# Kernel optimization log

Hardware: AMD Instinct MI355X
Metric: run time of the kernel (lower is better)

## Reference

```python
import jax, jax.numpy as jnp
import numpy as np

DIM = 2048
N_HEADS = 16
HEAD_DIM = DIM // N_HEADS
B, S = 2, 2048


def apply_rotary(x, cos, sin):
    # x: [..., dim]; cos/sin broadcast to [..., dim//2]
    # even/odd interleaved rotation, matching the torch ::2 / 1::2 indexing
    xe = x[..., 0::2]
    xo = x[..., 1::2]
    oe = xe * cos - xo * sin
    oo = xo * cos + xe * sin
    return jnp.stack([oe, oo], axis=-1).reshape(x.shape)


def setup_inputs() -> dict:
    key = jax.random.key(0)
    ks = jax.random.split(key, 12)
    scale = 1.0 / np.sqrt(DIM)
    x = jax.random.normal(ks[0], (B, S, DIM), dtype=jnp.float32)
    cos = jax.random.normal(ks[1], (S, DIM // 2), dtype=jnp.float32)
    sin = jax.random.normal(ks[2], (S, DIM // 2), dtype=jnp.float32)
    mask = jnp.zeros((1, 1, S, S), dtype=jnp.float32)
    Wq = jax.random.normal(ks[3], (DIM, DIM), dtype=jnp.float32) * scale
    bq = jnp.zeros((DIM,), dtype=jnp.float32)
    Wk = jax.random.normal(ks[4], (DIM, DIM), dtype=jnp.float32) * scale
    bk = jnp.zeros((DIM,), dtype=jnp.float32)
    Wv = jax.random.normal(ks[5], (DIM, DIM), dtype=jnp.float32) * scale
    bv = jnp.zeros((DIM,), dtype=jnp.float32)
    Wo = jax.random.normal(ks[6], (DIM, DIM), dtype=jnp.float32) * scale
    bo = jnp.zeros((DIM,), dtype=jnp.float32)
    return {"x": x, "cos": cos, "sin": sin, "mask": mask,
            "Wq": Wq, "bq": bq, "Wk": Wk, "bk": bk,
            "Wv": Wv, "bv": bv, "Wo": Wo, "bo": bo}


def reference(x, cos, sin, mask, Wq, bq, Wk, bk, Wv, bv, Wo, bo):
    # Linear projections (torch nn.Linear: y = x @ W.T + b)
    q = jnp.einsum('bsd,ed->bse', x, Wq) + bq
    k = jnp.einsum('bsd,ed->bse', x, Wk) + bk
    v = jnp.einsum('bsd,ed->bse', x, Wv) + bv
    # RoPE on full dim, then split into heads (faithful to source ordering)
    q = apply_rotary(q, cos, sin).reshape(B, S, N_HEADS, HEAD_DIM)
    k = apply_rotary(k, cos, sin).reshape(B, S, N_HEADS, HEAD_DIM)
    v = v.reshape(B, S, N_HEADS, HEAD_DIM)
    scale = 1.0 / jnp.sqrt(jnp.float32(HEAD_DIM))
    attn = jnp.einsum('bqhd,bkhd->bhqk', q, k) * scale  # [B,H,S,S]
    attn = attn + mask
    attn = jax.nn.softmax(attn, axis=-1)
    out = jnp.einsum('bhqk,bkhd->bqhd', attn, v).reshape(B, S, DIM)
    return jnp.einsum('bsd,ed->bse', out, Wo) + bo
```

## Files before the change

### kernel.cpp

```cpp
#include <hip/hip_runtime.h>

#define DIM   2048
#define SLEN  2048
#define BATCH 2
#define NHEAD 16
#define HDIM  128
#define MROWS (BATCH*SLEN)

typedef __attribute__((ext_vector_type(8))) __bf16 bf16x8;
typedef __attribute__((ext_vector_type(4))) float  f32x4;
typedef __attribute__((ext_vector_type(8))) unsigned short u16x8;
typedef __attribute__((ext_vector_type(4))) unsigned short u16x4;

__device__ __forceinline__ unsigned short f2bf(float f) {
  union { float f; unsigned u; } v; v.f = f;
  unsigned r = v.u + 0x7FFFu + ((v.u >> 16) & 1u);
  return (unsigned short)(r >> 16);
}
__device__ __forceinline__ float bf2f(unsigned short h) {
  union { unsigned u; float f; } v; v.u = ((unsigned)h) << 16;
  return v.f;
}
__device__ __forceinline__ void gload16(const void* g, void* l) {
  __builtin_amdgcn_global_load_lds(
      (const __attribute__((address_space(1))) void*)g,
      (__attribute__((address_space(3))) void*)l, 16, 0, 0);
}

__global__ __launch_bounds__(256) void conv_f32_bf16(
    const float* __restrict__ in, unsigned short* __restrict__ out, int n4) {
  int t = blockIdx.x * 256 + threadIdx.x;
  if (t >= n4) return;
  f32x4 v = *(const f32x4*)(in + (size_t)t * 4);
  u16x4 o;
  o[0] = f2bf(v[0]); o[1] = f2bf(v[1]); o[2] = f2bf(v[2]); o[3] = f2bf(v[3]);
  *(u16x4*)(out + (size_t)t * 4) = o;
}

template<int OUT_MODE>
__global__ __launch_bounds__(256) void gemm_bt(
    const unsigned short* __restrict__ A,
    const unsigned short* __restrict__ Bw,
    const float* __restrict__ bias,
    void* __restrict__ Cout, int M, int N, int K)
{
  __shared__ __align__(16) unsigned short As[128][32];
  __shared__ __align__(16) unsigned short Bs[128][32];
  const int tid  = threadIdx.x;
  const int lane = tid & 63;
  const int wid  = tid >> 6;
  const int wr   = wid >> 1, wc = wid & 1;
  const int lrow = lane >> 4, lcol = lane & 15;
  const int row0 = blockIdx.x * 128, col0 = blockIdx.y * 128;

  f32x4 acc[4][4] = {};

  const unsigned short* Ablk = A  + (size_t)row0 * K;
  const unsigned short* Bblk = Bw + (size_t)col0 * K;
  char* AsB = (char*)&As[0][0];
  char* BsB = (char*)&Bs[0][0];

  for (int k0 = 0; k0 < K; k0 += 32) {
#pragma unroll
    for (int r = 0; r < 2; ++r) {
      int f = r * 256 + tid;
      gload16(Ablk + (size_t)(f >> 2) * K + k0 + (f & 3) * 8, AsB + (r * 256 + wid * 64) * 16);
      gload16(Bblk + (size_t)(f >> 2) * K + k0 + (f & 3) * 8, BsB + (r * 256 + wid * 64) * 16);
    }
    __syncthreads();
    bf16x8 af[4], bfv[4];
#pragma unroll
    for (int m = 0; m < 4; ++m)
      af[m] = *(const bf16x8*)&As[wr * 64 + m * 16 + lcol][lrow * 8];
#pragma unroll
    for (int n = 0; n < 4; ++n)
      bfv[n] = *(const bf16x8*)&Bs[wc * 64 + n * 16 + lcol][lrow * 8];
#pragma unroll
    for (int m = 0; m < 4; ++m)
#pragma unroll
      for (int n = 0; n < 4; ++n)
        acc[m][n] = __builtin_amdgcn_mfma_f32_16x16x32_bf16(af[m], bfv[n], acc[m][n], 0, 0, 0);
    __syncthreads();
  }

#pragma unroll
  for (int m = 0; m < 4; ++m) {
#pragma unroll
    for (int n = 0; n < 4; ++n) {
      int col = col0 + wc * 64 + n * 16 + lcol;
      float bv = bias[col];
      if (OUT_MODE == 2) {
        int row = row0 + wr * 64 + m * 16 + lrow * 4;
        u16x4 o;
#pragma unroll
        for (int j = 0; j < 4; ++j) o[j] = f2bf(acc[m][n][j] + bv);
        *(u16x4*)((unsigned short*)Cout +
                  ((size_t)((row >> 11) * DIM + col)) * SLEN + (row & (SLEN - 1))) = o;
      } else {
#pragma unroll
        for (int j = 0; j < 4; ++j) {
          int row = row0 + wr * 64 + m * 16 + lrow * 4 + j;
          float val = acc[m][n][j] + bv;
          if (OUT_MODE == 1) ((unsigned short*)Cout)[(size_t)row * N + col] = f2bf(val);
          else               ((float*)Cout)[(size_t)row * N + col] = val;
        }
      }
    }
  }
}

__global__ __launch_bounds__(256) void rope_inplace(
    unsigned short* __restrict__ q,
    const float* __restrict__ cosT, const float* __restrict__ sinT, float scale) {
  int t   = blockIdx.x * 256 + threadIdx.x;
  int row = t >> 8;
  int e0  = (t & 255) * 8;
  int s   = row & (SLEN - 1);
  unsigned short* p = q + (size_t)row * DIM + e0;
  u16x8 v = *(u16x8*)p;
  f32x4 c  = *(const f32x4*)(cosT + (size_t)s * (DIM / 2) + (e0 >> 1));
  f32x4 sn = *(const f32x4*)(sinT + (size_t)s * (DIM / 2) + (e0 >> 1));
#pragma unroll
  for (int i = 0; i < 4; ++i) {
    float xe = bf2f(v[2 * i]), xo = bf2f(v[2 * i + 1]);
    float oe = (xe * c[i] - xo * sn[i]) * scale;
    float oo = (xo * c[i] + xe * sn[i]) * scale;
    v[2 * i] = f2bf(oe); v[2 * i + 1] = f2bf(oo);
  }
  *(u16x8*)p = v;
}

__global__ __launch_bounds__(256) void attn_fwd(
    const unsigned short* __restrict__ Q,
    const unsigned short* __restrict__ Kg,
    const unsigned short* __restrict__ VtG,
    const float* __restrict__ mask,
    unsigned short* __restrict__ O)
{
  __shared__ __align__(16) unsigned short Ks[64][128];
  __shared__ __align__(16) unsigned short Vts[128][64];
  __shared__ __align__(16) unsigned short Ps[4][16][64];

  const int qt = blockIdx.x, h = blockIdx.y, b = blockIdx.z;
  const int tid = threadIdx.x, lane = tid & 63, wid = tid >> 6;
  const int lrow = lane >> 4, lcol = lane & 15;
  const int sx = (lcol & 7) << 4;

  const unsigned short* Qb  = Q  + ((size_t)(b * SLEN + qt * 64)) * DIM + h * HDIM;
  const unsigned short* Kb  = Kg + (size_t)(b * SLEN) * DIM + h * HDIM;
  const unsigned short* Vtb = VtG + ((size_t)(b * DIM + h * HDIM)) * SLEN;
  const float* maskRow = mask + (size_t)(qt * 64 + wid * 16 + lcol) * SLEN;

  bf16x8 qf[4];
#pragma unroll
  for (int kk = 0; kk < 4; ++kk)
    qf[kk] = *(const bf16x8*)(Qb + (size_t)(wid * 16 + lcol) * DIM + kk * 32 + lrow * 8);

  float m_run = -1e30f, l_run = 0.f;
  f32x4 acc_o[8] = {};

  char* KsB  = (char*)&Ks[0][0];
  char* VtsB = (char*)&Vts[0][0];
  char* PsB  = (char*)&Ps[0][0][0];

  for (int kt = 0; kt < SLEN / 64; ++kt) {
    __syncthreads();
#pragma unroll
    for (int r = 0; r < 4; ++r) {
      int L = r * 256 + wid * 64 + lane;
      int krow = L >> 4, kc = (L & 15) ^ (krow & 7);
      gload16(Kb + (size_t)(kt * 64 + krow) * DIM + kc * 8,
              KsB + (size_t)(r * 256 + wid * 64) * 16);
    }
#pragma unroll
    for (int r = 0; r < 4; ++r) {
      int L = r * 256 + wid * 64 + lane;
      int d = L >> 3, vc = (L & 7) ^ (d & 7);
      gload16(Vtb + (size_t)d * SLEN + kt * 64 + vc * 8,
              VtsB + (size_t)(r * 256 + wid * 64) * 16);
    }
    __syncthreads();

    f32x4 sacc[4] = {};
#pragma unroll
    for (int kn = 0; kn < 4; ++kn)
#pragma unroll
      for (int kk = 0; kk < 4; ++kk) {
        bf16x8 kf = *(const bf16x8*)(KsB + (size_t)(kn * 16 + lcol) * 256
                                         + ((kk * 64 + lrow * 16) ^ sx));
        sacc[kn] = __builtin_amdgcn_mfma_f32_16x16x32_bf16(kf, qf[kk], sacc[kn], 0, 0, 0);
      }

    float sv[16];
#pragma unroll
    for (int kn = 0; kn < 4; ++kn) {
      f32x4 mv = *(const f32x4*)(maskRow + kt * 64 + kn * 16 + lrow * 4);
#pragma unroll
      for (int r = 0; r < 4; ++r) sv[kn * 4 + r] = sacc[kn][r] + mv[r];
    }

    float pmax = sv[0];
#pragma unroll
    for (int i = 1; i < 16; ++i) pmax = fmaxf(pmax, sv[i]);
    pmax = fmaxf(pmax, __shfl_xor(pmax, 16, 64));
    pmax = fmaxf(pmax, __shfl_xor(pmax, 32, 64));

    if (!__all(pmax - m_run <= 8.0f)) {
      float mnew = fmaxf(m_run, pmax);
      float alpha = __expf(m_run - mnew);
      m_run = mnew;
      l_run *= alpha;
      float ar[4];
#pragma unroll
      for (int r = 0; r < 4; ++r) ar[r] = __shfl(alpha, lrow * 4 + r, 64);
#pragma unroll
      for (int d = 0; d < 8; ++d) {
        f32x4 t = acc_o[d];
#pragma unroll
        for (int r = 0; r < 4; ++r) t[r] *= ar[r];
        acc_o[d] = t;
      }
    }

    float pv[16];
    float rsum = 0.f;
#pragma unroll
    for (int i = 0; i < 16; ++i) { float pe = __expf(sv[i] - m_run); pv[i] = pe; rsum += pe; }
    rsum += __shfl_xor(rsum, 16, 64);
    rsum += __shfl_xor(rsum, 32, 64);
    l_run += rsum;

#pragma unroll
    for (int kn = 0; kn < 4; ++kn)
#pragma unroll
      for (int r = 0; r < 4; ++r)
        *(unsigned short*)(PsB + wid * 2048 + lcol * 128
                           + ((kn * 32 + (lrow * 4 + r) * 2) ^ sx)) = f2bf(pv[kn * 4 + r]);

    bf16x8 pf[2];
#pragma unroll
    for (int ks = 0; ks < 2; ++ks)
      pf[ks] = *(const bf16x8*)(PsB + wid * 2048 + lcol * 128
                                + ((ks * 64 + lrow * 16) ^ sx));
#pragma unroll
    for (int d = 0; d < 8; ++d)
#pragma unroll
      for (int ks = 0; ks < 2; ++ks) {
        bf16x8 vf = *(const bf16x8*)(VtsB + (size_t)(d * 16 + lcol) * 128
                                          + ((ks * 64 + lrow * 16) ^ sx));
        acc_o[d] = __builtin_amdgcn_mfma_f32_16x16x32_bf16(pf[ks], vf, acc_o[d], 0, 0, 0);
      }
  }

  float linv[4];
#pragma unroll
  for (int r = 0; r < 4; ++r) linv[r] = 1.0f / __shfl(l_run, lrow * 4 + r, 64);
  int orow0 = b * SLEN + qt * 64 + wid * 16 + lrow * 4;
#pragma unroll
  for (int d = 0; d < 8; ++d)
#pragma unroll
    for (int r = 0; r < 4; ++r) {
      float o = acc_o[d][r] * linv[r];
      O[(size_t)(orow0 + r) * DIM + h * HDIM + d * 16 + lcol] = f2bf(o);
    }
}

extern "C" void kernel_launch(void* const* d_in, const int* in_sizes, int n_in,
                              void* d_out, int out_size, void* d_ws, size_t ws_size,
                              hipStream_t stream) {
  const float* x    = (const float*)d_in[0];
  const float* cosT = (const float*)d_in[1];
  const float* sinT = (const float*)d_in[2];
  const float* mask = (const float*)d_in[3];
  const float* Wq   = (const float*)d_in[4];
  const float* bq   = (const float*)d_in[5];
  const float* Wk   = (const float*)d_in[6];
  const float* bk   = (const float*)d_in[7];
  const float* Wv   = (const float*)d_in[8];
  const float* bv   = (const float*)d_in[9];
  const float* Wo   = (const float*)d_in[10];
  const float* bo   = (const float*)d_in[11];

  const size_t MB = 1u << 20;
  if (ws_size < 72 * MB) return;

  char* ws = (char*)d_ws;
  unsigned short* xb = (unsigned short*)(ws);
  unsigned short* qb = (unsigned short*)(ws + 16 * MB);
  unsigned short* kb = (unsigned short*)(ws + 32 * MB);
  unsigned short* Vt = (unsigned short*)(ws + 48 * MB);
  unsigned short* Wb = (unsigned short*)(ws + 64 * MB);
  unsigned short* Ob = xb;

  dim3 gGemm(MROWS / 128, DIM / 128);
  const float scale = 0.08838834764831845f;

  conv_f32_bf16<<<8192, 256, 0, stream>>>(x, xb, (MROWS * DIM) / 4);
  conv_f32_bf16<<<4096, 256, 0, stream>>>(Wq, Wb, (DIM * DIM) / 4);
  gemm_bt<1><<<gGemm, 256, 0, stream>>>(xb, Wb, bq, qb, MROWS, DIM, DIM);
  conv_f32_bf16<<<4096, 256, 0, stream>>>(Wk, Wb, (DIM * DIM) / 4);
  gemm_bt<1><<<gGemm, 256, 0, stream>>>(xb, Wb, bk, kb, MROWS, DIM, DIM);
  conv_f32_bf16<<<4096, 256, 0, stream>>>(Wv, Wb, (DIM * DIM) / 4);
  gemm_bt<2><<<gGemm, 256, 0, stream>>>(xb, Wb, bv, Vt, MROWS, DIM, DIM);
  rope_inplace<<<4096, 256, 0, stream>>>(qb, cosT, sinT, scale);
  rope_inplace<<<4096, 256, 0, stream>>>(kb, cosT, sinT, 1.0f);
  attn_fwd<<<dim3(SLEN / 64, NHEAD, BATCH), 256, 0, stream>>>(qb, kb, Vt, mask, Ob);
  conv_f32_bf16<<<4096, 256, 0, stream>>>(Wo, Wb, (DIM * DIM) / 4);
  gemm_bt<0><<<gGemm, 256, 0, stream>>>(Ob, Wb, bo, d_out, MROWS, DIM, DIM);
}
```

Baseline: 434.8 us.

## Process two 16-row query subtiles per wave in attention to reuse K/V tiles

Each wave in the attention kernel now handles 32 query rows as two 16-row subtiles, so every block covers 128 queries instead of 64 and the grid is halved. Each K and V fragment read from LDS feeds two MFMAs, which halves global K/V loads per query and LDS reads per MFMA. P stores to LDS are also vectorized into 4-element writes. The cost is roughly double the accumulator and softmax-state registers and fewer blocks, which may reduce occupancy (512 blocks on the GPU).

```diff
diff --git a/kernel.cpp b/kernel.cpp
--- a/kernel.cpp
+++ b/kernel.cpp
@@ -139,25 +139,27 @@
 {
   __shared__ __align__(16) unsigned short Ks[64][128];
   __shared__ __align__(16) unsigned short Vts[128][64];
-  __shared__ __align__(16) unsigned short Ps[4][16][64];
+  __shared__ __align__(16) unsigned short Ps[4][32][64];
 
   const int qt = blockIdx.x, h = blockIdx.y, b = blockIdx.z;
   const int tid = threadIdx.x, lane = tid & 63, wid = tid >> 6;
   const int lrow = lane >> 4, lcol = lane & 15;
   const int sx = (lcol & 7) << 4;
 
-  const unsigned short* Qb  = Q  + ((size_t)(b * SLEN + qt * 64)) * DIM + h * HDIM;
+  const unsigned short* Qb  = Q  + ((size_t)(b * SLEN + qt * 128 + wid * 32)) * DIM + h * HDIM;
   const unsigned short* Kb  = Kg + (size_t)(b * SLEN) * DIM + h * HDIM;
   const unsigned short* Vtb = VtG + ((size_t)(b * DIM + h * HDIM)) * SLEN;
-  const float* maskRow = mask + (size_t)(qt * 64 + wid * 16 + lcol) * SLEN;
-
-  bf16x8 qf[4];
-#pragma unroll
-  for (int kk = 0; kk < 4; ++kk)
-    qf[kk] = *(const bf16x8*)(Qb + (size_t)(wid * 16 + lcol) * DIM + kk * 32 + lrow * 8);
-
-  float m_run = -1e30f, l_run = 0.f;
-  f32x4 acc_o[8] = {};
+  const float* mrow0 = mask + (size_t)(qt * 128 + wid * 32 + lcol) * SLEN;
+
+  bf16x8 qf[2][4];
+#pragma unroll
+  for (int qs = 0; qs < 2; ++qs)
+#pragma unroll
+    for (int kk = 0; kk < 4; ++kk)
+      qf[qs][kk] = *(const bf16x8*)(Qb + (size_t)(qs * 16 + lcol) * DIM + kk * 32 + lrow * 8);
+
+  float m_run[2] = {-1e30f, -1e30f}, l_run[2] = {0.f, 0.f};
+  f32x4 acc_o[2][8] = {};
 
   char* KsB  = (char*)&Ks[0][0];
   char* VtsB = (char*)&Vts[0][0];
@@ -181,88 +183,100 @@
     }
     __syncthreads();
 
-    f32x4 sacc[4] = {};
+    f32x4 sacc[2][4] = {};
 #pragma unroll
     for (int kn = 0; kn < 4; ++kn)
 #pragma unroll
       for (int kk = 0; kk < 4; ++kk) {
         bf16x8 kf = *(const bf16x8*)(KsB + (size_t)(kn * 16 + lcol) * 256
                                          + ((kk * 64 + lrow * 16) ^ sx));
-        sacc[kn] = __builtin_amdgcn_mfma_f32_16x16x32_bf16(kf, qf[kk], sacc[kn], 0, 0, 0);
-      }
-
-    float sv[16];
-#pragma unroll
-    for (int kn = 0; kn < 4; ++kn) {
-      f32x4 mv = *(const f32x4*)(maskRow + kt * 64 + kn * 16 + lrow * 4);
-#pragma unroll
-      for (int r = 0; r < 4; ++r) sv[kn * 4 + r] = sacc[kn][r] + mv[r];
-    }
-
-    float pmax = sv[0];
-#pragma unroll
-    for (int i = 1; i < 16; ++i) pmax = fmaxf(pmax, sv[i]);
-    pmax = fmaxf(pmax, __shfl_xor(pmax, 16, 64));
-    pmax = fmaxf(pmax, __shfl_xor(pmax, 32, 64));
-
-    if (!__all(pmax - m_run <= 8.0f)) {
-      float mnew = fmaxf(m_run, pmax);
-      float alpha = __expf(m_run - mnew);
-      m_run = mnew;
-      l_run *= alpha;
-      float ar[4];
-#pragma unroll
-      for (int r = 0; r < 4; ++r) ar[r] = __shfl(alpha, lrow * 4 + r, 64);
-#pragma unroll
-      for (int d = 0; d < 8; ++d) {
-        f32x4 t = acc_o[d];
-#pragma unroll
-        for (int r = 0; r < 4; ++r) t[r] *= ar[r];
-        acc_o[d] = t;
-      }
-    }
-
-    float pv[16];
-    float rsum = 0.f;
-#pragma unroll
-    for (int i = 0; i < 16; ++i) { float pe = __expf(sv[i] - m_run); pv[i] = pe; rsum += pe; }
-    rsum += __shfl_xor(rsum, 16, 64);
-    rsum += __shfl_xor(rsum, 32, 64);
-    l_run += rsum;
-
-#pragma unroll
-    for (int kn = 0; kn < 4; ++kn)
-#pragma unroll
-      for (int r = 0; r < 4; ++r)
-        *(unsigned short*)(PsB + wid * 2048 + lcol * 128
-                           + ((kn * 32 + (lrow * 4 + r) * 2) ^ sx)) = f2bf(pv[kn * 4 + r]);
-
-    bf16x8 pf[2];
-#pragma unroll
-    for (int ks = 0; ks < 2; ++ks)
-      pf[ks] = *(const bf16x8*)(PsB + wid * 2048 + lcol * 128
-                                + ((ks * 64 + lrow * 16) ^ sx));
+        sacc[0][kn] = __builtin_amdgcn_mfma_f32_16x16x32_bf16(kf, qf[0][kk], sacc[0][kn], 0, 0, 0);
+        sacc[1][kn] = __builtin_amdgcn_mfma_f32_16x16x32_bf16(kf, qf[1][kk], sacc[1][kn], 0, 0, 0);
+      }
+
+#pragma unroll
+    for (int qs = 0; qs < 2; ++qs) {
+      float sv[16];
+#pragma unroll
+      for (int kn = 0; kn < 4; ++kn) {
+        f32x4 mv = *(const f32x4*)(mrow0 + (size_t)qs * 16 * SLEN + kt * 64 + kn * 16 + lrow * 4);
+#pragma unroll
+        for (int r = 0; r < 4; ++r) sv[kn * 4 + r] = sacc[qs][kn][r] + mv[r];
+      }
+
+      float pmax = sv[0];
+#pragma unroll
+      for (int i = 1; i < 16; ++i) pmax = fmaxf(pmax, sv[i]);
+      pmax = fmaxf(pmax, __shfl_xor(pmax, 16, 64));
+      pmax = fmaxf(pmax, __shfl_xor(pmax, 32, 64));
+
+      if (!__all(pmax - m_run[qs] <= 8.0f)) {
+        float mnew = fmaxf(m_run[qs], pmax);
+        float alpha = __expf(m_run[qs] - mnew);
+        m_run[qs] = mnew;
+        l_run[qs] *= alpha;
+        float ar[4];
+#pragma unroll
+        for (int r = 0; r < 4; ++r) ar[r] = __shfl(alpha, lrow * 4 + r, 64);
+#pragma unroll
+        for (int d = 0; d < 8; ++d) {
+          f32x4 t = acc_o[qs][d];
+#pragma unroll
+          for (int r = 0; r < 4; ++r) t[r] *= ar[r];
+          acc_o[qs][d] = t;
+        }
+      }
+
+      float pv[16];
+      float rsum = 0.f;
+#pragma unroll
+      for (int i = 0; i < 16; ++i) { float pe = __expf(sv[i] - m_run[qs]); pv[i] = pe; rsum += pe; }
+      rsum += __shfl_xor(rsum, 16, 64);
+      rsum += __shfl_xor(rsum, 32, 64);
+      l_run[qs] += rsum;
+
+#pragma unroll
+      for (int kn = 0; kn < 4; ++kn) {
+        u16x4 o;
+#pragma unroll
+        for (int r = 0; r < 4; ++r) o[r] = f2bf(pv[kn * 4 + r]);
+        *(u16x4*)(PsB + wid * 4096 + (qs * 16 + lcol) * 128
+                  + ((kn * 32 + lrow * 8) ^ sx)) = o;
+      }
+    }
+
+    bf16x8 pf[2][2];
+#pragma unroll
+    for (int qs = 0; qs < 2; ++qs)
+#pragma unroll
+      for (int ks = 0; ks < 2; ++ks)
+        pf[qs][ks] = *(const bf16x8*)(PsB + wid * 4096 + (qs * 16 + lcol) * 128
+                                      + ((ks * 64 + lrow * 16) ^ sx));
 #pragma unroll
     for (int d = 0; d < 8; ++d)
 #pragma unroll
       for (int ks = 0; ks < 2; ++ks) {
         bf16x8 vf = *(const bf16x8*)(VtsB + (size_t)(d * 16 + lcol) * 128
                                           + ((ks * 64 + lrow * 16) ^ sx));
-        acc_o[d] = __builtin_amdgcn_mfma_f32_16x16x32_bf16(pf[ks], vf, acc_o[d], 0, 0, 0);
-      }
-  }
-
-  float linv[4];
-#pragma unroll
-  for (int r = 0; r < 4; ++r) linv[r] = 1.0f / __shfl(l_run, lrow * 4 + r, 64);
-  int orow0 = b * SLEN + qt * 64 + wid * 16 + lrow * 4;
-#pragma unroll
-  for (int d = 0; d < 8; ++d)
-#pragma unroll
-    for (int r = 0; r < 4; ++r) {
-      float o = acc_o[d][r] * linv[r];
-      O[(size_t)(orow0 + r) * DIM + h * HDIM + d * 16 + lcol] = f2bf(o);
-    }
+        acc_o[0][d] = __builtin_amdgcn_mfma_f32_16x16x32_bf16(pf[0][ks], vf, acc_o[0][d], 0, 0, 0);
+        acc_o[1][d] = __builtin_amdgcn_mfma_f32_16x16x32_bf16(pf[1][ks], vf, acc_o[1][d], 0, 0, 0);
+      }
+  }
+
+#pragma unroll
+  for (int qs = 0; qs < 2; ++qs) {
+    float linv[4];
+#pragma unroll
+    for (int r = 0; r < 4; ++r) linv[r] = 1.0f / __shfl(l_run[qs], lrow * 4 + r, 64);
+    int orow0 = b * SLEN + qt * 128 + wid * 32 + qs * 16 + lrow * 4;
+#pragma unroll
+    for (int d = 0; d < 8; ++d)
+#pragma unroll
+      for (int r = 0; r < 4; ++r) {
+        float o = acc_o[qs][d][r] * linv[r];
+        O[(size_t)(orow0 + r) * DIM + h * HDIM + d * 16 + lcol] = f2bf(o);
+      }
+  }
 }
 
 extern "C" void kernel_launch(void* const* d_in, const int* in_sizes, int n_in,
@@ -304,7 +318,7 @@
   gemm_bt<2><<<gGemm, 256, 0, stream>>>(xb, Wb, bv, Vt, MROWS, DIM, DIM);
   rope_inplace<<<4096, 256, 0, stream>>>(qb, cosT, sinT, scale);
   rope_inplace<<<4096, 256, 0, stream>>>(kb, cosT, sinT, 1.0f);
-  attn_fwd<<<dim3(SLEN / 64, NHEAD, BATCH), 256, 0, stream>>>(qb, kb, Vt, mask, Ob);
+  attn_fwd<<<dim3(SLEN / 128, NHEAD, BATCH), 256, 0, stream>>>(qb, kb, Vt, mask, Ob);
   conv_f32_bf16<<<4096, 256, 0, stream>>>(Wo, Wb, (DIM * DIM) / 4);
   gemm_bt<0><<<gGemm, 256, 0, stream>>>(Ob, Wb, bo, d_out, MROWS, DIM, DIM);
 }
```

After: 466.4 us. 7.3% more time.
